# Kernel tuning notes

Measured on AMD Instinct MI355X. Metric: run time of the kernel, lower is better.

Reference implementation:

```python
import jax, jax.numpy as jnp
import numpy as np

N_NODES = 100000
N_EDGES = 6400000
D = 12

def setup_inputs() -> dict:
    key = jax.random.key(0)
    k1, k2, k3, k4 = jax.random.split(key, 4)
    x = jax.random.normal(k1, (N_NODES, D), dtype=jnp.float32)
    W_l = jax.random.normal(k2, (D, D), dtype=jnp.float32) / np.sqrt(D)
    W_r = jax.random.normal(k3, (D, D), dtype=jnp.float32) / np.sqrt(D)
    b = jnp.zeros((D,), dtype=jnp.float32)
    edge_index = jax.random.randint(k4, (2, N_EDGES), 0, N_NODES, dtype=jnp.int64)
    return {"x": x, "W_l": W_l, "W_r": W_r, "b": b, "edge_index": edge_index}

def reference(x, W_l, W_r, b, edge_index):
    # PyG SAGEConv (mean aggregation): out = lin_l(mean_{j in N(i)} x_j) + lin_r(x_i)
    src = edge_index[0]
    dst = edge_index[1]
    n = x.shape[0]
    msgs = x[src]                                      # [E, D] gather
    agg = jax.ops.segment_sum(msgs, dst, num_segments=n)          # [N, D]
    cnt = jax.ops.segment_sum(jnp.ones_like(dst, dtype=x.dtype), dst, num_segments=n)
    mean = agg / jnp.maximum(cnt, 1.0)[:, None]        # [N, D]
    out = mean @ W_l.T + x @ W_r.T + b                 # lin_l carries the bias in PyG
    return out
```

## Files before the change

### kernel.cpp

```cpp
#include <hip/hip_runtime.h>

#define N_NODES 100000
#define N_EDGES 6400000
#define D 12

#define SLOG 5
#define SSZ  32
#define NB   ((N_NODES + SSZ - 1) / SSZ)
#define NBLK 512
#define EPB  ((N_EDGES + NBLK - 1) / NBLK)
#define RSTR 13

#define CAP  1280
#define EPT  (CAP / 256)

__device__ __forceinline__ unsigned int f2bf(float f) {
    unsigned int u = __float_as_uint(f);
    return (u + 0x7fffu + ((u >> 16) & 1u)) >> 16;
}
__device__ __forceinline__ unsigned int pk2(float lo, float hi) {
    return (f2bf(hi) << 16) | f2bf(lo);
}
__device__ __forceinline__ float bflo(unsigned int u) { return __uint_as_float(u << 16); }
__device__ __forceinline__ float bfhi(unsigned int u) { return __uint_as_float(u & 0xffff0000u); }

__global__ __launch_bounds__(256) void prep_kernel(
    const float* __restrict__ x, unsigned int* __restrict__ xb)
{
    int i = blockIdx.x * 256 + threadIdx.x;
    if (i >= N_NODES) return;
    const float4* xr = (const float4*)(x) + (size_t)i * 3;
    float4 a = xr[0], b = xr[1], c = xr[2];
    unsigned int* o = xb + (size_t)i * 8;
    ((uint4*)o)[0] = make_uint4(pk2(a.x, a.y), pk2(a.z, a.w), pk2(b.x, b.y), pk2(b.z, b.w));
    ((uint2*)(o + 4))[0] = make_uint2(pk2(c.x, c.y), pk2(c.z, c.w));
}

__global__ __launch_bounds__(256) void hist_kernel(
    const int* __restrict__ ei, int* __restrict__ bins)
{
    __shared__ int h[NB];
    for (int i = threadIdx.x; i < NB; i += 256) h[i] = 0;
    __syncthreads();
    const int* dei = ei + N_EDGES;
    int start = blockIdx.x * EPB;
    int end = min(start + EPB, N_EDGES);
    int e = start + (int)threadIdx.x;
    while (e + 768 < end) {
        int d0 = dei[e], d1 = dei[e + 256], d2 = dei[e + 512], d3 = dei[e + 768];
        atomicAdd(&h[d0 >> SLOG], 1);
        atomicAdd(&h[d1 >> SLOG], 1);
        atomicAdd(&h[d2 >> SLOG], 1);
        atomicAdd(&h[d3 >> SLOG], 1);
        e += 1024;
    }
    while (e < end) { atomicAdd(&h[dei[e] >> SLOG], 1); e += 256; }
    __syncthreads();
    for (int i = threadIdx.x; i < NB; i += 256) {
        int c = h[i];
        if (c) atomicAdd(&bins[i], c);
    }
}

__global__ __launch_bounds__(1024) void scan_kernel(
    const int* __restrict__ bins, int* __restrict__ base, int* __restrict__ cursor)
{
    __shared__ int buf[1024];
    __shared__ int carry;
    int tid = threadIdx.x;
    if (tid == 0) carry = 0;
    __syncthreads();
    for (int c0 = 0; c0 < NB; c0 += 1024) {
        int i = c0 + tid;
        int v = (i < NB) ? bins[i] : 0;
        buf[tid] = v;
        __syncthreads();
        for (int o = 1; o < 1024; o <<= 1) {
            int t = (tid >= o) ? buf[tid - o] : 0;
            __syncthreads();
            buf[tid] += t;
            __syncthreads();
        }
        int excl = buf[tid] - v + carry;
        if (i < NB) { base[i] = excl; cursor[i] = excl; }
        __syncthreads();
        if (tid == 0) carry += buf[1023];
        __syncthreads();
    }
    if (tid == 0) base[NB] = N_EDGES;
}

__global__ __launch_bounds__(256) void scatter_sort_kernel(
    const int* __restrict__ ei, int* __restrict__ cursor,
    unsigned int* __restrict__ sorted)
{
    __shared__ int h[NB];
    for (int i = threadIdx.x; i < NB; i += 256) h[i] = 0;
    __syncthreads();
    const int* dei = ei + N_EDGES;
    int start = blockIdx.x * EPB;
    int end = min(start + EPB, N_EDGES);
    int e = start + (int)threadIdx.x;
    while (e + 768 < end) {
        int d0 = dei[e], d1 = dei[e + 256], d2 = dei[e + 512], d3 = dei[e + 768];
        atomicAdd(&h[d0 >> SLOG], 1);
        atomicAdd(&h[d1 >> SLOG], 1);
        atomicAdd(&h[d2 >> SLOG], 1);
        atomicAdd(&h[d3 >> SLOG], 1);
        e += 1024;
    }
    while (e < end) { atomicAdd(&h[dei[e] >> SLOG], 1); e += 256; }
    __syncthreads();
    for (int i = threadIdx.x; i < NB; i += 256) {
        int c = h[i];
        h[i] = c ? atomicAdd(&cursor[i], c) : 0;
    }
    __syncthreads();
    e = start + (int)threadIdx.x;
    while (e + 768 < end) {
        int s0 = ei[e], s1 = ei[e + 256], s2 = ei[e + 512], s3 = ei[e + 768];
        int d0 = dei[e], d1 = dei[e + 256], d2 = dei[e + 512], d3 = dei[e + 768];
        int p0 = atomicAdd(&h[d0 >> SLOG], 1);
        int p1 = atomicAdd(&h[d1 >> SLOG], 1);
        int p2 = atomicAdd(&h[d2 >> SLOG], 1);
        int p3 = atomicAdd(&h[d3 >> SLOG], 1);
        sorted[p0] = ((unsigned)s0 << SLOG) | (unsigned)(d0 & (SSZ - 1));
        sorted[p1] = ((unsigned)s1 << SLOG) | (unsigned)(d1 & (SSZ - 1));
        sorted[p2] = ((unsigned)s2 << SLOG) | (unsigned)(d2 & (SSZ - 1));
        sorted[p3] = ((unsigned)s3 << SLOG) | (unsigned)(d3 & (SSZ - 1));
        e += 1024;
    }
    while (e < end) {
        int s = ei[e], d = dei[e];
        int pos = atomicAdd(&h[d >> SLOG], 1);
        sorted[pos] = ((unsigned)s << SLOG) | (unsigned)(d & (SSZ - 1));
        e += 256;
    }
}

__global__ __launch_bounds__(256, 4) void agg_finalize_kernel(
    const unsigned int* __restrict__ sorted, const int* __restrict__ base,
    const unsigned int* __restrict__ xb,
    const float* __restrict__ x, const float* __restrict__ Wl,
    const float* __restrict__ Wr, const float* __restrict__ bias,
    float* __restrict__ out)
{
    __shared__ float sWl[D * D], sWr[D * D], sb[D];
    __shared__ int cnt[SSZ];
    __shared__ int segbase[SSZ + 1];
    __shared__ int cursor[SSZ];
    __shared__ int cnt_tot[SSZ];
    __shared__ unsigned vals[CAP * 6];

    int t = threadIdx.x;
    int b = blockIdx.x;

    if (t < D * D) { sWl[t] = Wl[t]; sWr[t] = Wr[t]; }
    if (t < D) sb[t] = bias[t];
    if (t < SSZ) cnt_tot[t] = 0;

    float acc[D];
#pragma unroll
    for (int d = 0; d < D; ++d) acc[d] = 0.f;

    int loc = t >> 3;
    int sub = t & 7;

    int start = base[b];
    int end = base[b + 1];

    for (int c0 = start; c0 < end; c0 += CAP) {
        int n = min(CAP, end - c0);
        if (t < SSZ) cnt[t] = 0;
        __syncthreads();

        unsigned pe[EPT];
        int ne = 0;
        for (int j = t; j < n; j += 256) pe[ne++] = sorted[c0 + j];
#pragma unroll
        for (int k = 0; k < EPT; ++k)
            if (k < ne) atomicAdd(&cnt[pe[k] & (SSZ - 1)], 1);
        __syncthreads();

        if (t == 0) {
            int s = 0;
#pragma unroll
            for (int i = 0; i < SSZ; ++i) { segbase[i] = s; s += cnt[i]; }
            segbase[SSZ] = s;
        }
        __syncthreads();
        if (t < SSZ) { cursor[t] = segbase[t]; cnt_tot[t] += cnt[t]; }
        __syncthreads();

#pragma unroll
        for (int k = 0; k < EPT; ++k) {
            if (k < ne) {
                unsigned p = pe[k];
                int slot = atomicAdd(&cursor[p & (SSZ - 1)], 1);
                const unsigned* r = xb + (size_t)(p >> SLOG) * 8;
                uint2 q0 = ((const uint2*)r)[0];
                uint2 q1 = ((const uint2*)r)[1];
                uint2 q2 = ((const uint2*)r)[2];
                unsigned* vv = &vals[slot * 6];
                ((uint2*)vv)[0] = q0;
                ((uint2*)vv)[1] = q1;
                ((uint2*)vv)[2] = q2;
            }
        }
        __syncthreads();

        int s0 = segbase[loc], s1 = segbase[loc + 1];
        for (int j = s0 + sub; j < s1; j += 8) {
            const unsigned* vv = &vals[j * 6];
            uint2 q0 = ((const uint2*)vv)[0];
            uint2 q1 = ((const uint2*)vv)[1];
            uint2 q2 = ((const uint2*)vv)[2];
            acc[0]  += bflo(q0.x); acc[1]  += bfhi(q0.x);
            acc[2]  += bflo(q0.y); acc[3]  += bfhi(q0.y);
            acc[4]  += bflo(q1.x); acc[5]  += bfhi(q1.x);
            acc[6]  += bflo(q1.y); acc[7]  += bfhi(q1.y);
            acc[8]  += bflo(q2.x); acc[9]  += bfhi(q2.x);
            acc[10] += bflo(q2.y); acc[11] += bfhi(q2.y);
        }
        __syncthreads();
    }

    float* red = (float*)vals;
#pragma unroll
    for (int d = 0; d < D; ++d) red[sub * 417 + loc * 13 + d] = acc[d];
    __syncthreads();

    if (t < SSZ) {
        int node = b * SSZ + t;
        float m[D];
#pragma unroll
        for (int d = 0; d < D; ++d) {
            float s = 0.f;
#pragma unroll
            for (int ss = 0; ss < 8; ++ss) s += red[ss * 417 + t * 13 + d];
            m[d] = s;
        }
        float inv = 1.f / fmaxf((float)cnt_tot[t], 1.f);
#pragma unroll
        for (int d = 0; d < D; ++d) m[d] *= inv;

        float xi[D];
        const float4* xr = (const float4*)(x) + (size_t)node * 3;
        float4 x0 = xr[0], x1 = xr[1], x2 = xr[2];
        xi[0] = x0.x; xi[1] = x0.y; xi[2]  = x0.z; xi[3]  = x0.w;
        xi[4] = x1.x; xi[5] = x1.y; xi[6]  = x1.z; xi[7]  = x1.w;
        xi[8] = x2.x; xi[9] = x2.y; xi[10] = x2.z; xi[11] = x2.w;

        float o[D];
#pragma unroll
        for (int oo = 0; oo < D; ++oo) {
            float a = sb[oo];
#pragma unroll
            for (int d = 0; d < D; ++d) {
                a += m[d] * sWl[oo * D + d];
                a += xi[d] * sWr[oo * D + d];
            }
            o[oo] = a;
        }
        float4* orow = (float4*)(out) + (size_t)node * 3;
        orow[0] = make_float4(o[0], o[1], o[2], o[3]);
        orow[1] = make_float4(o[4], o[5], o[6], o[7]);
        orow[2] = make_float4(o[8], o[9], o[10], o[11]);
    }
}

__global__ __launch_bounds__(256) void agg_finalize_f32_kernel(
    const unsigned int* __restrict__ sorted, const int* __restrict__ base,
    const float* __restrict__ x, const float* __restrict__ Wl,
    const float* __restrict__ Wr, const float* __restrict__ bias,
    float* __restrict__ out)
{
    __shared__ float agg[SSZ * RSTR];
    __shared__ float sWl[D * D], sWr[D * D], sb[D];
    int t = threadIdx.x;
    int b = blockIdx.x;
    for (int i = t; i < SSZ * RSTR; i += 256) agg[i] = 0.f;
    if (t < D * D) { sWl[t] = Wl[t]; sWr[t] = Wr[t]; }
    if (t < D) sb[t] = bias[t];
    __syncthreads();
    int start = base[b];
    int end = base[b + 1];
    for (int e = start + t; e < end; e += 256) {
        unsigned p = sorted[e];
        int src = (int)(p >> SLOG);
        int lc = (int)(p & (SSZ - 1));
        const float4* xr = (const float4*)(x) + (size_t)src * 3;
        float4 a = xr[0], b4 = xr[1], c = xr[2];
        float* ar = &agg[lc * RSTR];
        atomicAdd(ar + 0,  a.x);  atomicAdd(ar + 1,  a.y);
        atomicAdd(ar + 2,  a.z);  atomicAdd(ar + 3,  a.w);
        atomicAdd(ar + 4,  b4.x); atomicAdd(ar + 5,  b4.y);
        atomicAdd(ar + 6,  b4.z); atomicAdd(ar + 7,  b4.w);
        atomicAdd(ar + 8,  c.x);  atomicAdd(ar + 9,  c.y);
        atomicAdd(ar + 10, c.z);  atomicAdd(ar + 11, c.w);
        atomicAdd(ar + 12, 1.f);
    }
    __syncthreads();
    if (t < SSZ) {
        int node = b * SSZ + t;
        const float* ar = &agg[t * RSTR];
        float inv = 1.f / fmaxf(ar[12], 1.f);
        float m[D], xi[D];
#pragma unroll
        for (int d = 0; d < D; ++d) m[d] = ar[d] * inv;
        const float4* xr = (const float4*)(x) + (size_t)node * 3;
        float4 x0 = xr[0], x1 = xr[1], x2 = xr[2];
        xi[0] = x0.x; xi[1] = x0.y; xi[2]  = x0.z; xi[3]  = x0.w;
        xi[4] = x1.x; xi[5] = x1.y; xi[6]  = x1.z; xi[7]  = x1.w;
        xi[8] = x2.x; xi[9] = x2.y; xi[10] = x2.z; xi[11] = x2.w;
        float o[D];
#pragma unroll
        for (int oo = 0; oo < D; ++oo) {
            float a = sb[oo];
#pragma unroll
            for (int d = 0; d < D; ++d) {
                a += m[d] * sWl[oo * D + d];
                a += xi[d] * sWr[oo * D + d];
            }
            o[oo] = a;
        }
        float4* orow = (float4*)(out) + (size_t)node * 3;
        orow[0] = make_float4(o[0], o[1], o[2], o[3]);
        orow[1] = make_float4(o[4], o[5], o[6], o[7]);
        orow[2] = make_float4(o[8], o[9], o[10], o[11]);
    }
}


__global__ __launch_bounds__(256) void scatter_kernel(
    const int* __restrict__ ei, const float* __restrict__ x,
    float* __restrict__ agg, float* __restrict__ cnt)
{
    int e = blockIdx.x * blockDim.x + threadIdx.x;
    if (e >= N_EDGES) return;
    int src = ei[e];
    int dst = ei[N_EDGES + e];
    const float4* xr = (const float4*)(x + (size_t)src * D);
    float4 a = xr[0], b4 = xr[1], c = xr[2];
    float* dr = agg + (size_t)dst * D;
    atomicAdd(dr + 0,  a.x);  atomicAdd(dr + 1,  a.y);
    atomicAdd(dr + 2,  a.z);  atomicAdd(dr + 3,  a.w);
    atomicAdd(dr + 4,  b4.x); atomicAdd(dr + 5,  b4.y);
    atomicAdd(dr + 6,  b4.z); atomicAdd(dr + 7,  b4.w);
    atomicAdd(dr + 8,  c.x);  atomicAdd(dr + 9,  c.y);
    atomicAdd(dr + 10, c.z);  atomicAdd(dr + 11, c.w);
    atomicAdd(cnt + dst, 1.0f);
}

__global__ __launch_bounds__(256) void finalize_kernel(
    const float* __restrict__ x, const float* __restrict__ Wl,
    const float* __restrict__ Wr, const float* __restrict__ bias,
    const float* __restrict__ agg, const float* __restrict__ cnt,
    float* __restrict__ out)
{
    __shared__ float sWl[D * D], sWr[D * D], sb[D];
    int t = threadIdx.x;
    if (t < D * D) { sWl[t] = Wl[t]; sWr[t] = Wr[t]; }
    if (t < D) sb[t] = bias[t];
    __syncthreads();
    int i = blockIdx.x * blockDim.x + t;
    if (i >= N_NODES) return;
    float inv = 1.0f / fmaxf(cnt[i], 1.0f);
    float m[D], xi[D];
    const float4* ar = (const float4*)(agg + (size_t)i * D);
    const float4* xr = (const float4*)(x + (size_t)i * D);
    float4 a0 = ar[0], a1 = ar[1], a2 = ar[2];
    float4 x0 = xr[0], x1 = xr[1], x2 = xr[2];
    m[0] = a0.x * inv; m[1] = a0.y * inv; m[2]  = a0.z * inv; m[3]  = a0.w * inv;
    m[4] = a1.x * inv; m[5] = a1.y * inv; m[6]  = a1.z * inv; m[7]  = a1.w * inv;
    m[8] = a2.x * inv; m[9] = a2.y * inv; m[10] = a2.z * inv; m[11] = a2.w * inv;
    xi[0] = x0.x; xi[1] = x0.y; xi[2]  = x0.z; xi[3]  = x0.w;
    xi[4] = x1.x; xi[5] = x1.y; xi[6]  = x1.z; xi[7]  = x1.w;
    xi[8] = x2.x; xi[9] = x2.y; xi[10] = x2.z; xi[11] = x2.w;
    float o[D];
#pragma unroll
    for (int oo = 0; oo < D; ++oo) {
        float acc = sb[oo];
#pragma unroll
        for (int d = 0; d < D; ++d) {
            acc += m[d] * sWl[oo * D + d];
            acc += xi[d] * sWr[oo * D + d];
        }
        o[oo] = acc;
    }
    float4* orow = (float4*)(out + (size_t)i * D);
    orow[0] = make_float4(o[0], o[1], o[2], o[3]);
    orow[1] = make_float4(o[4], o[5], o[6], o[7]);
    orow[2] = make_float4(o[8], o[9], o[10], o[11]);
}

extern "C" void kernel_launch(void* const* d_in, const int* in_sizes, int n_in,
                              void* d_out, int out_size, void* d_ws, size_t ws_size,
                              hipStream_t stream) {
    const float* x    = (const float*)d_in[0];
    const float* Wl   = (const float*)d_in[1];
    const float* Wr   = (const float*)d_in[2];
    const float* bias = (const float*)d_in[3];
    const int*   ei   = (const int*)d_in[4];
    float* out = (float*)d_out;

    size_t sortedBytes = (size_t)N_EDGES * sizeof(unsigned int);
    size_t xbBytes     = (size_t)N_NODES * 8 * sizeof(unsigned int);
    size_t binsBytes   = (size_t)NB * sizeof(int);
    size_t baseBytes   = (size_t)(NB + 1) * sizeof(int);
    size_t neededFull = sortedBytes + xbBytes + binsBytes + baseBytes + binsBytes;
    size_t neededMid  = sortedBytes + binsBytes + baseBytes + binsBytes;

    if (ws_size >= neededFull) {
        char* p = (char*)d_ws;
        unsigned int* sorted = (unsigned int*)p;        p += sortedBytes;
        unsigned int* xb     = (unsigned int*)p;        p += xbBytes;
        int* bins   = (int*)p;                          p += binsBytes;
        int* base   = (int*)p;                          p += baseBytes;
        int* cursor = (int*)p;

        hipMemsetAsync(bins, 0, binsBytes, stream);
        prep_kernel<<<(N_NODES + 255) / 256, 256, 0, stream>>>(x, xb);
        hist_kernel<<<NBLK, 256, 0, stream>>>(ei, bins);
        scan_kernel<<<1, 1024, 0, stream>>>(bins, base, cursor);
        scatter_sort_kernel<<<NBLK, 256, 0, stream>>>(ei, cursor, sorted);
        agg_finalize_kernel<<<NB, 256, 0, stream>>>(sorted, base, xb, x, Wl, Wr, bias, out);
    } else if (ws_size >= neededMid) {
        char* p = (char*)d_ws;
        unsigned int* sorted = (unsigned int*)p;        p += sortedBytes;
        int* bins   = (int*)p;                          p += binsBytes;
        int* base   = (int*)p;                          p += baseBytes;
        int* cursor = (int*)p;

        hipMemsetAsync(bins, 0, binsBytes, stream);
        hist_kernel<<<NBLK, 256, 0, stream>>>(ei, bins);
        scan_kernel<<<1, 1024, 0, stream>>>(bins, base, cursor);
        scatter_sort_kernel<<<NBLK, 256, 0, stream>>>(ei, cursor, sorted);
        agg_finalize_f32_kernel<<<NB, 256, 0, stream>>>(sorted, base, x, Wl, Wr, bias, out);
    } else {
        float* agg = (float*)d_ws;
        float* cnt = agg + (size_t)N_NODES * D;
        hipMemsetAsync(d_ws, 0, ((size_t)N_NODES * D + N_NODES) * sizeof(float), stream);
        scatter_kernel<<<(N_EDGES + 255) / 256, 256, 0, stream>>>(ei, x, agg, cnt);
        finalize_kernel<<<(N_NODES + 255) / 256, 256, 0, stream>>>(x, Wl, Wr, bias, agg, cnt, out);
    }
}
```

Measured before the change: 308.3 us.

## Aggregate 128-node buckets with LDS float atomics and prefetch the next edge

Node buckets grow from 32 to 128 nodes, so each bucket kernel covers more nodes and more edges. The per-chunk local counting sort (count, prefix scan, scatter into LDS, then segmented reduction) is replaced by direct LDS float atomicAdds into a per-bucket accumulator, with the in-degree count kept in the 13th slot. A register double-buffer prefetches the next edge's bf16 row while the current one is accumulated, and a node bounds check is added because 128 does not divide the node count. This removes several barriers and the LDS staging per chunk, at the cost of 13 LDS atomics per edge and possible contention on shared slots. The larger bucket size also changes the histogram, scan and scatter-sort stages.

```diff
diff --git a/kernel.cpp b/kernel.cpp
--- a/kernel.cpp
+++ b/kernel.cpp
@@ -4,15 +4,12 @@
 #define N_EDGES 6400000
 #define D 12
 
-#define SLOG 5
-#define SSZ  32
+#define SLOG 7
+#define SSZ  128
 #define NB   ((N_NODES + SSZ - 1) / SSZ)
 #define NBLK 512
 #define EPB  ((N_EDGES + NBLK - 1) / NBLK)
 #define RSTR 13
-
-#define CAP  1280
-#define EPT  (CAP / 256)
 
 __device__ __forceinline__ unsigned int f2bf(float f) {
     unsigned int u = __float_as_uint(f);
@@ -138,134 +135,91 @@
     }
 }
 
-__global__ __launch_bounds__(256, 4) void agg_finalize_kernel(
+__global__ __launch_bounds__(256) void agg_bucket_kernel(
     const unsigned int* __restrict__ sorted, const int* __restrict__ base,
     const unsigned int* __restrict__ xb,
     const float* __restrict__ x, const float* __restrict__ Wl,
     const float* __restrict__ Wr, const float* __restrict__ bias,
     float* __restrict__ out)
 {
+    __shared__ float agg[SSZ * RSTR];
     __shared__ float sWl[D * D], sWr[D * D], sb[D];
-    __shared__ int cnt[SSZ];
-    __shared__ int segbase[SSZ + 1];
-    __shared__ int cursor[SSZ];
-    __shared__ int cnt_tot[SSZ];
-    __shared__ unsigned vals[CAP * 6];
 
     int t = threadIdx.x;
     int b = blockIdx.x;
 
+    for (int i = t; i < SSZ * RSTR; i += 256) agg[i] = 0.f;
     if (t < D * D) { sWl[t] = Wl[t]; sWr[t] = Wr[t]; }
     if (t < D) sb[t] = bias[t];
-    if (t < SSZ) cnt_tot[t] = 0;
-
-    float acc[D];
-#pragma unroll
-    for (int d = 0; d < D; ++d) acc[d] = 0.f;
-
-    int loc = t >> 3;
-    int sub = t & 7;
+    __syncthreads();
 
     int start = base[b];
     int end = base[b + 1];
 
-    for (int c0 = start; c0 < end; c0 += CAP) {
-        int n = min(CAP, end - c0);
-        if (t < SSZ) cnt[t] = 0;
-        __syncthreads();
-
-        unsigned pe[EPT];
-        int ne = 0;
-        for (int j = t; j < n; j += 256) pe[ne++] = sorted[c0 + j];
-#pragma unroll
-        for (int k = 0; k < EPT; ++k)
-            if (k < ne) atomicAdd(&cnt[pe[k] & (SSZ - 1)], 1);
-        __syncthreads();
-
-        if (t == 0) {
-            int s = 0;
-#pragma unroll
-            for (int i = 0; i < SSZ; ++i) { segbase[i] = s; s += cnt[i]; }
-            segbase[SSZ] = s;
+    int e = start + t;
+    unsigned p = 0;
+    uint4 q01 = make_uint4(0, 0, 0, 0);
+    uint2 q2 = make_uint2(0, 0);
+    if (e < end) {
+        p = sorted[e];
+        const unsigned* r = xb + (size_t)(p >> SLOG) * 8;
+        q01 = ((const uint4*)r)[0];
+        q2  = ((const uint2*)(r + 4))[0];
+    }
+    while (e < end) {
+        int e2 = e + 256;
+        unsigned p2 = 0;
+        uint4 n01 = make_uint4(0, 0, 0, 0);
+        uint2 n2 = make_uint2(0, 0);
+        if (e2 < end) {
+            p2 = sorted[e2];
+            const unsigned* r2 = xb + (size_t)(p2 >> SLOG) * 8;
+            n01 = ((const uint4*)r2)[0];
+            n2  = ((const uint2*)(r2 + 4))[0];
         }
-        __syncthreads();
-        if (t < SSZ) { cursor[t] = segbase[t]; cnt_tot[t] += cnt[t]; }
-        __syncthreads();
-
-#pragma unroll
-        for (int k = 0; k < EPT; ++k) {
-            if (k < ne) {
-                unsigned p = pe[k];
-                int slot = atomicAdd(&cursor[p & (SSZ - 1)], 1);
-                const unsigned* r = xb + (size_t)(p >> SLOG) * 8;
-                uint2 q0 = ((const uint2*)r)[0];
-                uint2 q1 = ((const uint2*)r)[1];
-                uint2 q2 = ((const uint2*)r)[2];
-                unsigned* vv = &vals[slot * 6];
-                ((uint2*)vv)[0] = q0;
-                ((uint2*)vv)[1] = q1;
-                ((uint2*)vv)[2] = q2;
-            }
-        }
-        __syncthreads();
-
-        int s0 = segbase[loc], s1 = segbase[loc + 1];
-        for (int j = s0 + sub; j < s1; j += 8) {
-            const unsigned* vv = &vals[j * 6];
-            uint2 q0 = ((const uint2*)vv)[0];
-            uint2 q1 = ((const uint2*)vv)[1];
-            uint2 q2 = ((const uint2*)vv)[2];
-            acc[0]  += bflo(q0.x); acc[1]  += bfhi(q0.x);
-            acc[2]  += bflo(q0.y); acc[3]  += bfhi(q0.y);
-            acc[4]  += bflo(q1.x); acc[5]  += bfhi(q1.x);
-            acc[6]  += bflo(q1.y); acc[7]  += bfhi(q1.y);
-            acc[8]  += bflo(q2.x); acc[9]  += bfhi(q2.x);
-            acc[10] += bflo(q2.y); acc[11] += bfhi(q2.y);
-        }
-        __syncthreads();
-    }
-
-    float* red = (float*)vals;
-#pragma unroll
-    for (int d = 0; d < D; ++d) red[sub * 417 + loc * 13 + d] = acc[d];
+        float* ar = &agg[(p & (SSZ - 1)) * RSTR];
+        atomicAdd(ar + 0,  bflo(q01.x)); atomicAdd(ar + 1,  bfhi(q01.x));
+        atomicAdd(ar + 2,  bflo(q01.y)); atomicAdd(ar + 3,  bfhi(q01.y));
+        atomicAdd(ar + 4,  bflo(q01.z)); atomicAdd(ar + 5,  bfhi(q01.z));
+        atomicAdd(ar + 6,  bflo(q01.w)); atomicAdd(ar + 7,  bfhi(q01.w));
+        atomicAdd(ar + 8,  bflo(q2.x));  atomicAdd(ar + 9,  bfhi(q2.x));
+        atomicAdd(ar + 10, bflo(q2.y));  atomicAdd(ar + 11, bfhi(q2.y));
+        atomicAdd(ar + 12, 1.f);
+        e = e2; p = p2; q01 = n01; q2 = n2;
+    }
     __syncthreads();
 
     if (t < SSZ) {
         int node = b * SSZ + t;
-        float m[D];
-#pragma unroll
-        for (int d = 0; d < D; ++d) {
-            float s = 0.f;
-#pragma unroll
-            for (int ss = 0; ss < 8; ++ss) s += red[ss * 417 + t * 13 + d];
-            m[d] = s;
+        if (node < N_NODES) {
+            const float* ar = &agg[t * RSTR];
+            float inv = 1.f / fmaxf(ar[12], 1.f);
+            float m[D], xi[D];
+#pragma unroll
+            for (int d = 0; d < D; ++d) m[d] = ar[d] * inv;
+
+            const float4* xr = (const float4*)(x) + (size_t)node * 3;
+            float4 x0 = xr[0], x1 = xr[1], x2 = xr[2];
+            xi[0] = x0.x; xi[1] = x0.y; xi[2]  = x0.z; xi[3]  = x0.w;
+            xi[4] = x1.x; xi[5] = x1.y; xi[6]  = x1.z; xi[7]  = x1.w;
+            xi[8] = x2.x; xi[9] = x2.y; xi[10] = x2.z; xi[11] = x2.w;
+
+            float o[D];
+#pragma unroll
+            for (int oo = 0; oo < D; ++oo) {
+                float a = sb[oo];
+#pragma unroll
+                for (int d = 0; d < D; ++d) {
+                    a += m[d] * sWl[oo * D + d];
+                    a += xi[d] * sWr[oo * D + d];
+                }
+                o[oo] = a;
+            }
+            float4* orow = (float4*)(out) + (size_t)node * 3;
+            orow[0] = make_float4(o[0], o[1], o[2], o[3]);
+            orow[1] = make_float4(o[4], o[5], o[6], o[7]);
+            orow[2] = make_float4(o[8], o[9], o[10], o[11]);
         }
-        float inv = 1.f / fmaxf((float)cnt_tot[t], 1.f);
-#pragma unroll
-        for (int d = 0; d < D; ++d) m[d] *= inv;
-
-        float xi[D];
-        const float4* xr = (const float4*)(x) + (size_t)node * 3;
-        float4 x0 = xr[0], x1 = xr[1], x2 = xr[2];
-        xi[0] = x0.x; xi[1] = x0.y; xi[2]  = x0.z; xi[3]  = x0.w;
-        xi[4] = x1.x; xi[5] = x1.y; xi[6]  = x1.z; xi[7]  = x1.w;
-        xi[8] = x2.x; xi[9] = x2.y; xi[10] = x2.z; xi[11] = x2.w;
-
-        float o[D];
-#pragma unroll
-        for (int oo = 0; oo < D; ++oo) {
-            float a = sb[oo];
-#pragma unroll
-            for (int d = 0; d < D; ++d) {
-                a += m[d] * sWl[oo * D + d];
-                a += xi[d] * sWr[oo * D + d];
-            }
-            o[oo] = a;
-        }
-        float4* orow = (float4*)(out) + (size_t)node * 3;
-        orow[0] = make_float4(o[0], o[1], o[2], o[3]);
-        orow[1] = make_float4(o[4], o[5], o[6], o[7]);
-        orow[2] = make_float4(o[8], o[9], o[10], o[11]);
     }
 }
 
@@ -303,31 +257,33 @@
     __syncthreads();
     if (t < SSZ) {
         int node = b * SSZ + t;
-        const float* ar = &agg[t * RSTR];
-        float inv = 1.f / fmaxf(ar[12], 1.f);
-        float m[D], xi[D];
-#pragma unroll
-        for (int d = 0; d < D; ++d) m[d] = ar[d] * inv;
-        const float4* xr = (const float4*)(x) + (size_t)node * 3;
-        float4 x0 = xr[0], x1 = xr[1], x2 = xr[2];
-        xi[0] = x0.x; xi[1] = x0.y; xi[2]  = x0.z; xi[3]  = x0.w;
-        xi[4] = x1.x; xi[5] = x1.y; xi[6]  = x1.z; xi[7]  = x1.w;
-        xi[8] = x2.x; xi[9] = x2.y; xi[10] = x2.z; xi[11] = x2.w;
-        float o[D];
-#pragma unroll
-        for (int oo = 0; oo < D; ++oo) {
-            float a = sb[oo];
-#pragma unroll
-            for (int d = 0; d < D; ++d) {
-                a += m[d] * sWl[oo * D + d];
-                a += xi[d] * sWr[oo * D + d];
+        if (node < N_NODES) {
+            const float* ar = &agg[t * RSTR];
+            float inv = 1.f / fmaxf(ar[12], 1.f);
+            float m[D], xi[D];
+#pragma unroll
+            for (int d = 0; d < D; ++d) m[d] = ar[d] * inv;
+            const float4* xr = (const float4*)(x) + (size_t)node * 3;
+            float4 x0 = xr[0], x1 = xr[1], x2 = xr[2];
+            xi[0] = x0.x; xi[1] = x0.y; xi[2]  = x0.z; xi[3]  = x0.w;
+            xi[4] = x1.x; xi[5] = x1.y; xi[6]  = x1.z; xi[7]  = x1.w;
+            xi[8] = x2.x; xi[9] = x2.y; xi[10] = x2.z; xi[11] = x2.w;
+            float o[D];
+#pragma unroll
+            for (int oo = 0; oo < D; ++oo) {
+                float a = sb[oo];
+#pragma unroll
+                for (int d = 0; d < D; ++d) {
+                    a += m[d] * sWl[oo * D + d];
+                    a += xi[d] * sWr[oo * D + d];
+                }
+                o[oo] = a;
             }
-            o[oo] = a;
+            float4* orow = (float4*)(out) + (size_t)node * 3;
+            orow[0] = make_float4(o[0], o[1], o[2], o[3]);
+            orow[1] = make_float4(o[4], o[5], o[6], o[7]);
+            orow[2] = make_float4(o[8], o[9], o[10], o[11]);
         }
-        float4* orow = (float4*)(out) + (size_t)node * 3;
-        orow[0] = make_float4(o[0], o[1], o[2], o[3]);
-        orow[1] = make_float4(o[4], o[5], o[6], o[7]);
-        orow[2] = make_float4(o[8], o[9], o[10], o[11]);
     }
 }
 
@@ -424,7 +380,7 @@
         hist_kernel<<<NBLK, 256, 0, stream>>>(ei, bins);
         scan_kernel<<<1, 1024, 0, stream>>>(bins, base, cursor);
         scatter_sort_kernel<<<NBLK, 256, 0, stream>>>(ei, cursor, sorted);
-        agg_finalize_kernel<<<NB, 256, 0, stream>>>(sorted, base, xb, x, Wl, Wr, bias, out);
+        agg_bucket_kernel<<<NB, 256, 0, stream>>>(sorted, base, xb, x, Wl, Wr, bias, out);
     } else if (ws_size >= neededMid) {
         char* p = (char*)d_ws;
         unsigned int* sorted = (unsigned int*)p;        p += sortedBytes;
```

New measurement: 764.0 us. 2.48x slower.

## Widen destination buckets to 128 nodes with two threads per node and parallel scan

Applied to the files above, without the earlier changes.

Raises the bucket size from 32 to 128 destination nodes and the per-chunk capacity from 1280 to 2048 edges, so there are fewer buckets and fewer blocks. Each node is now reduced by 2 threads instead of 8, which shrinks the cross-thread reduction. The serial single-thread prefix over the segment counts is replaced by a parallel scan. Bounds checks are added because 100000 is not a multiple of 128. In exchange, shared memory per block grows, the 4-blocks-per-CU launch bound is dropped, and high-degree nodes see longer serial accumulation per thread.

```diff
diff --git a/kernel.cpp b/kernel.cpp
--- a/kernel.cpp
+++ b/kernel.cpp
@@ -4,14 +4,14 @@
 #define N_EDGES 6400000
 #define D 12
 
-#define SLOG 5
-#define SSZ  32
+#define SLOG 7
+#define SSZ  128
 #define NB   ((N_NODES + SSZ - 1) / SSZ)
 #define NBLK 512
 #define EPB  ((N_EDGES + NBLK - 1) / NBLK)
 #define RSTR 13
 
-#define CAP  1280
+#define CAP  2048
 #define EPT  (CAP / 256)
 
 __device__ __forceinline__ unsigned int f2bf(float f) {
@@ -138,7 +138,7 @@
     }
 }
 
-__global__ __launch_bounds__(256, 4) void agg_finalize_kernel(
+__global__ __launch_bounds__(256) void agg_reg_kernel(
     const unsigned int* __restrict__ sorted, const int* __restrict__ base,
     const unsigned int* __restrict__ xb,
     const float* __restrict__ x, const float* __restrict__ Wl,
@@ -147,6 +147,7 @@
 {
     __shared__ float sWl[D * D], sWr[D * D], sb[D];
     __shared__ int cnt[SSZ];
+    __shared__ int sbuf[SSZ];
     __shared__ int segbase[SSZ + 1];
     __shared__ int cursor[SSZ];
     __shared__ int cnt_tot[SSZ];
@@ -163,8 +164,8 @@
 #pragma unroll
     for (int d = 0; d < D; ++d) acc[d] = 0.f;
 
-    int loc = t >> 3;
-    int sub = t & 7;
+    int loc = t >> 1;
+    int sub = t & 1;
 
     int start = base[b];
     int end = base[b + 1];
@@ -182,11 +183,17 @@
             if (k < ne) atomicAdd(&cnt[pe[k] & (SSZ - 1)], 1);
         __syncthreads();
 
-        if (t == 0) {
-            int s = 0;
-#pragma unroll
-            for (int i = 0; i < SSZ; ++i) { segbase[i] = s; s += cnt[i]; }
-            segbase[SSZ] = s;
+        if (t < SSZ) sbuf[t] = cnt[t];
+        __syncthreads();
+        for (int o = 1; o < SSZ; o <<= 1) {
+            int v = (t < SSZ && t >= o) ? sbuf[t - o] : 0;
+            __syncthreads();
+            if (t < SSZ) sbuf[t] += v;
+            __syncthreads();
+        }
+        if (t < SSZ) {
+            segbase[t + 1] = sbuf[t];
+            if (t == 0) segbase[0] = 0;
         }
         __syncthreads();
         if (t < SSZ) { cursor[t] = segbase[t]; cnt_tot[t] += cnt[t]; }
@@ -210,7 +217,7 @@
         __syncthreads();
 
         int s0 = segbase[loc], s1 = segbase[loc + 1];
-        for (int j = s0 + sub; j < s1; j += 8) {
+        for (int j = s0 + sub; j < s1; j += 2) {
             const unsigned* vv = &vals[j * 6];
             uint2 q0 = ((const uint2*)vv)[0];
             uint2 q1 = ((const uint2*)vv)[1];
@@ -227,45 +234,43 @@
 
     float* red = (float*)vals;
 #pragma unroll
-    for (int d = 0; d < D; ++d) red[sub * 417 + loc * 13 + d] = acc[d];
+    for (int d = 0; d < D; ++d) red[sub * 1664 + loc * 13 + d] = acc[d];
     __syncthreads();
 
     if (t < SSZ) {
         int node = b * SSZ + t;
-        float m[D];
-#pragma unroll
-        for (int d = 0; d < D; ++d) {
-            float s = 0.f;
-#pragma unroll
-            for (int ss = 0; ss < 8; ++ss) s += red[ss * 417 + t * 13 + d];
-            m[d] = s;
-        }
-        float inv = 1.f / fmaxf((float)cnt_tot[t], 1.f);
-#pragma unroll
-        for (int d = 0; d < D; ++d) m[d] *= inv;
-
-        float xi[D];
-        const float4* xr = (const float4*)(x) + (size_t)node * 3;
-        float4 x0 = xr[0], x1 = xr[1], x2 = xr[2];
-        xi[0] = x0.x; xi[1] = x0.y; xi[2]  = x0.z; xi[3]  = x0.w;
-        xi[4] = x1.x; xi[5] = x1.y; xi[6]  = x1.z; xi[7]  = x1.w;
-        xi[8] = x2.x; xi[9] = x2.y; xi[10] = x2.z; xi[11] = x2.w;
-
-        float o[D];
-#pragma unroll
-        for (int oo = 0; oo < D; ++oo) {
-            float a = sb[oo];
-#pragma unroll
-            for (int d = 0; d < D; ++d) {
-                a += m[d] * sWl[oo * D + d];
-                a += xi[d] * sWr[oo * D + d];
+        if (node < N_NODES) {
+            float m[D];
+#pragma unroll
+            for (int d = 0; d < D; ++d)
+                m[d] = red[t * 13 + d] + red[1664 + t * 13 + d];
+            float inv = 1.f / fmaxf((float)cnt_tot[t], 1.f);
+#pragma unroll
+            for (int d = 0; d < D; ++d) m[d] *= inv;
+
+            float xi[D];
+            const float4* xr = (const float4*)(x) + (size_t)node * 3;
+            float4 x0 = xr[0], x1 = xr[1], x2 = xr[2];
+            xi[0] = x0.x; xi[1] = x0.y; xi[2]  = x0.z; xi[3]  = x0.w;
+            xi[4] = x1.x; xi[5] = x1.y; xi[6]  = x1.z; xi[7]  = x1.w;
+            xi[8] = x2.x; xi[9] = x2.y; xi[10] = x2.z; xi[11] = x2.w;
+
+            float o[D];
+#pragma unroll
+            for (int oo = 0; oo < D; ++oo) {
+                float a = sb[oo];
+#pragma unroll
+                for (int d = 0; d < D; ++d) {
+                    a += m[d] * sWl[oo * D + d];
+                    a += xi[d] * sWr[oo * D + d];
+                }
+                o[oo] = a;
             }
-            o[oo] = a;
-        }
-        float4* orow = (float4*)(out) + (size_t)node * 3;
-        orow[0] = make_float4(o[0], o[1], o[2], o[3]);
-        orow[1] = make_float4(o[4], o[5], o[6], o[7]);
-        orow[2] = make_float4(o[8], o[9], o[10], o[11]);
+            float4* orow = (float4*)(out) + (size_t)node * 3;
+            orow[0] = make_float4(o[0], o[1], o[2], o[3]);
+            orow[1] = make_float4(o[4], o[5], o[6], o[7]);
+            orow[2] = make_float4(o[8], o[9], o[10], o[11]);
+        }
     }
 }
 
@@ -303,31 +308,33 @@
     __syncthreads();
     if (t < SSZ) {
         int node = b * SSZ + t;
-        const float* ar = &agg[t * RSTR];
-        float inv = 1.f / fmaxf(ar[12], 1.f);
-        float m[D], xi[D];
-#pragma unroll
-        for (int d = 0; d < D; ++d) m[d] = ar[d] * inv;
-        const float4* xr = (const float4*)(x) + (size_t)node * 3;
-        float4 x0 = xr[0], x1 = xr[1], x2 = xr[2];
-        xi[0] = x0.x; xi[1] = x0.y; xi[2]  = x0.z; xi[3]  = x0.w;
-        xi[4] = x1.x; xi[5] = x1.y; xi[6]  = x1.z; xi[7]  = x1.w;
-        xi[8] = x2.x; xi[9] = x2.y; xi[10] = x2.z; xi[11] = x2.w;
-        float o[D];
-#pragma unroll
-        for (int oo = 0; oo < D; ++oo) {
-            float a = sb[oo];
-#pragma unroll
-            for (int d = 0; d < D; ++d) {
-                a += m[d] * sWl[oo * D + d];
-                a += xi[d] * sWr[oo * D + d];
+        if (node < N_NODES) {
+            const float* ar = &agg[t * RSTR];
+            float inv = 1.f / fmaxf(ar[12], 1.f);
+            float m[D], xi[D];
+#pragma unroll
+            for (int d = 0; d < D; ++d) m[d] = ar[d] * inv;
+            const float4* xr = (const float4*)(x) + (size_t)node * 3;
+            float4 x0 = xr[0], x1 = xr[1], x2 = xr[2];
+            xi[0] = x0.x; xi[1] = x0.y; xi[2]  = x0.z; xi[3]  = x0.w;
+            xi[4] = x1.x; xi[5] = x1.y; xi[6]  = x1.z; xi[7]  = x1.w;
+            xi[8] = x2.x; xi[9] = x2.y; xi[10] = x2.z; xi[11] = x2.w;
+            float o[D];
+#pragma unroll
+            for (int oo = 0; oo < D; ++oo) {
+                float a = sb[oo];
+#pragma unroll
+                for (int d = 0; d < D; ++d) {
+                    a += m[d] * sWl[oo * D + d];
+                    a += xi[d] * sWr[oo * D + d];
+                }
+                o[oo] = a;
             }
-            o[oo] = a;
-        }
-        float4* orow = (float4*)(out) + (size_t)node * 3;
-        orow[0] = make_float4(o[0], o[1], o[2], o[3]);
-        orow[1] = make_float4(o[4], o[5], o[6], o[7]);
-        orow[2] = make_float4(o[8], o[9], o[10], o[11]);
+            float4* orow = (float4*)(out) + (size_t)node * 3;
+            orow[0] = make_float4(o[0], o[1], o[2], o[3]);
+            orow[1] = make_float4(o[4], o[5], o[6], o[7]);
+            orow[2] = make_float4(o[8], o[9], o[10], o[11]);
+        }
     }
 }
 
@@ -410,6 +417,7 @@
     size_t baseBytes   = (size_t)(NB + 1) * sizeof(int);
     size_t neededFull = sortedBytes + xbBytes + binsBytes + baseBytes + binsBytes;
     size_t neededMid  = sortedBytes + binsBytes + baseBytes + binsBytes;
+    size_t neededLast = ((size_t)N_NODES * D + N_NODES) * sizeof(float);
 
     if (ws_size >= neededFull) {
         char* p = (char*)d_ws;
@@ -424,7 +432,7 @@
         hist_kernel<<<NBLK, 256, 0, stream>>>(ei, bins);
         scan_kernel<<<1, 1024, 0, stream>>>(bins, base, cursor);
         scatter_sort_kernel<<<NBLK, 256, 0, stream>>>(ei, cursor, sorted);
-        agg_finalize_kernel<<<NB, 256, 0, stream>>>(sorted, base, xb, x, Wl, Wr, bias, out);
+        agg_reg_kernel<<<NB, 256, 0, stream>>>(sorted, base, xb, x, Wl, Wr, bias, out);
     } else if (ws_size >= neededMid) {
         char* p = (char*)d_ws;
         unsigned int* sorted = (unsigned int*)p;        p += sortedBytes;
@@ -440,7 +448,7 @@
     } else {
         float* agg = (float*)d_ws;
         float* cnt = agg + (size_t)N_NODES * D;
-        hipMemsetAsync(d_ws, 0, ((size_t)N_NODES * D + N_NODES) * sizeof(float), stream);
+        hipMemsetAsync(d_ws, 0, neededLast, stream);
         scatter_kernel<<<(N_EDGES + 255) / 256, 256, 0, stream>>>(ei, x, agg, cnt);
         finalize_kernel<<<(N_NODES + 255) / 256, 256, 0, stream>>>(x, Wl, Wr, bias, agg, cnt, out);
     }
```

Result: faster. 276.9 us (-10.2%).
